# Performance work log

Measured on AMD Instinct MI355X. Metric: run time of the kernel, lower is better.

## Reference

```python
import jax, jax.numpy as jnp
import numpy as np

N_ITEMS = 100001  # n_items + 1 (padding idx 0)
D = 128           # item_embedding_dim == hidden_size
P = 3             # purposes
S, B = 100, 256   # seq_len, batch
TAU = 0.1
EPS = 0.01


def setup_inputs() -> dict:
    key = jax.random.key(0)
    ks = jax.random.split(key, 6)
    std = 1.0 / np.sqrt(D)
    seq = jax.random.randint(ks[0], (S, B), 0, N_ITEMS)          # [S, B] item ids
    lens = jax.random.randint(ks[1], (B,), 1, S + 1)             # valid lengths in [1, S]
    emb_table = jax.random.uniform(ks[2], (N_ITEMS, D), minval=-std, maxval=std, dtype=jnp.float32)
    purpose_table = jax.random.uniform(ks[3], (P, D), minval=-std, maxval=std, dtype=jnp.float32)
    x2h_w = jax.random.uniform(ks[4], (P, 3 * D, D), minval=-std, maxval=std, dtype=jnp.float32)  # 3 cells
    h2h_w = jax.random.uniform(ks[5], (P, 3 * D, D), minval=-std, maxval=std, dtype=jnp.float32)
    return {"seq": seq, "lens": lens, "emb_table": emb_table,
            "purpose_table": purpose_table, "x2h_w": x2h_w, "h2h_w": h2h_w}


def _psru_cell(x, h, concen, Wx, Wh):
    # x: [B,D], h: [B,D], concen: [B], Wx/Wh: [3D, D]
    gx = x @ Wx.T                              # [B, 3D]
    gh = h @ Wh.T                              # [B, 3D]
    i_r, i_i, i_n = jnp.split(gx, 3, axis=1)
    h_r, h_i, h_n = jnp.split(gh, 3, axis=1)
    resetgate = jax.nn.sigmoid(i_r + h_r)
    inputgate = jax.nn.sigmoid(i_i + h_i)
    newgate = jnp.tanh(i_n + resetgate * h_n)
    multi = jnp.where(concen >= EPS, concen, 0.0)[:, None] * inputgate
    return h + multi * (newgate - h)


def reference(seq, lens, emb_table, purpose_table, x2h_w, h2h_w):
    # padding_idx = 0
    emb_table = emb_table.at[0].set(0.0)
    # concentration matrix: softmax over purposes of normalized-embedding similarity / tau
    item_n = emb_table / jnp.clip(jnp.linalg.norm(emb_table, axis=1, keepdims=True), 1e-12)
    attr_n = purpose_table / jnp.clip(jnp.linalg.norm(purpose_table, axis=1, keepdims=True), 1e-12)
    g = jax.nn.softmax((item_n @ attr_n.T) / TAU, axis=1)   # [V, P]  (exp/sum == softmax)
    g = g.at[0].set(0.0)

    embs = emb_table[seq]        # [S, B, D]
    g_seq = g[seq]               # [S, B, P]

    h0 = jnp.zeros((P, B, D), emb_table.dtype)

    def step(h, xs):
        x, gq = xs  # x: [B,D], gq: [B,P]
        h_new = jnp.stack([_psru_cell(x, h[p], gq[:, p], x2h_w[p], h2h_w[p]) for p in range(P)])
        return h_new, h_new

    _, hs = jax.lax.scan(step, h0, (embs, g_seq))            # hs: [S, P, B, D]

    # select hidden at last valid step per example: outs[lens-1, arange(B)]
    h_last = hs[lens - 1, :, jnp.arange(B), :]               # [B, P, D]

    # delta_c[b,v] = sum_p g[v,p] * <h_last[b,p], item_n[v]>  (== original VC_cand * item_embs sum)
    logits = sum((h_last[:, p, :] @ item_n.T) * g[None, :, p] for p in range(P))  # [B, V]
    return jax.nn.sigmoid(logits)
```

## Files before the change

### kernel.cpp

```cpp
#include <hip/hip_runtime.h>
#include <hip/hip_bf16.h>
#include <math.h>

#define N_ITEMS 100001
#define DIM 128
#define NP 3
#define SEQ 100
#define NB 256
#define G3 384
#define TAU 0.1f
#define EPS_C 0.01f

#define OFF_G     0
#define OFF_C     300016
#define OFF_WXT   600032
#define OFF_WHT   747488
#define OFF_HLAST 894944
#define OFF_GX    993248
#define WS_FLOATS_PATHA (993248 + 29491200)

typedef float f32x4 __attribute__((ext_vector_type(4)));
typedef short s16x8 __attribute__((ext_vector_type(8)));
typedef unsigned int u32x4 __attribute__((ext_vector_type(4)));

__device__ __forceinline__ float sigmoidf_fast(float x) {
    return __builtin_amdgcn_rcpf(1.f + __builtin_amdgcn_exp2f(-1.4426950408889634f * x));
}
__device__ __forceinline__ float tanhf_fast(float x) {
    return 1.f - 2.f * __builtin_amdgcn_rcpf(1.f + __builtin_amdgcn_exp2f(2.8853900817779268f * x));
}
__device__ __forceinline__ unsigned short f2bf(float x) {
    union { float f; unsigned u; } v; v.f = x;
    unsigned r = v.u + 0x7fffu + ((v.u >> 16) & 1u);
    return (unsigned short)(r >> 16);
}
__device__ __forceinline__ float bf2f(unsigned short h) {
    union { unsigned u; float f; } v; v.u = ((unsigned)h) << 16;
    return v.f;
}
__device__ __forceinline__ unsigned cvt_pk_bf16(float a, float b) {
    unsigned r;
    asm("v_cvt_pk_bf16_f32 %0, %1, %2" : "=v"(r) : "v"(a), "v"(b));
    return r;
}

__global__ void k_prep_w(const float* __restrict__ x2h, const float* __restrict__ h2h,
                         float* __restrict__ wxT, float* __restrict__ whT) {
    int idx = blockIdx.x * 256 + threadIdx.x;
    if (idx >= NP * DIM * G3) return;
    int j = idx % G3;
    int k = (idx / G3) % DIM;
    int p = idx / (G3 * DIM);
    wxT[idx] = x2h[((size_t)p * G3 + j) * DIM + k];
    whT[idx] = h2h[((size_t)p * G3 + j) * DIM + k];
}

__global__ __launch_bounds__(256) void k_prep_wA(const float* __restrict__ x2h,
                                                 const float* __restrict__ h2h,
                                                 short* __restrict__ wxA_hi,
                                                 short* __restrict__ wxA_lo,
                                                 short* __restrict__ whA_hi,
                                                 short* __restrict__ whA_lo) {
    int e = blockIdx.x * 256 + threadIdx.x;
    if (e >= 2 * NP * 24 * 4 * 64) return;
    int which = (e >= NP * 24 * 4 * 64);
    int f = which ? e - NP * 24 * 4 * 64 : e;
    const float* tab = which ? h2h : x2h;
    short* dh = which ? whA_hi : wxA_hi;
    short* dl = which ? whA_lo : wxA_lo;
    int lane = f & 63;
    int ks = (f >> 6) & 3;
    int mt = (f >> 8) % 24;
    int p  = f / 6144;
    int j = mt * 16 + (lane & 15);
    int d = ks * 32 + (lane >> 4) * 8;
    const float* src = tab + ((size_t)p * G3 + j) * DIM + d;
    short hi[8], lo[8];
#pragma unroll
    for (int u = 0; u < 8; ++u) {
        float x = src[u];
        unsigned short h = f2bf(x);
        hi[u] = (short)h;
        lo[u] = (short)f2bf(x - bf2f(h));
    }
    *(s16x8*)(dh + (size_t)f * 8) = *(const s16x8*)hi;
    *(s16x8*)(dl + (size_t)f * 8) = *(const s16x8*)lo;
}

__global__ __launch_bounds__(256) void k_gc(const float* __restrict__ emb,
                                            const float* __restrict__ pt,
                                            float* __restrict__ g, float* __restrict__ c) {
    __shared__ float pt_l[G3];
    __shared__ float ainv[NP];
    int tid = threadIdx.x;
    for (int u = tid; u < G3; u += 256) pt_l[u] = pt[u];
    __syncthreads();
    if (tid < NP) {
        float ss = 0.f;
        for (int k = 0; k < DIM; ++k) { float v = pt_l[tid * DIM + k]; ss += v * v; }
        ainv[tid] = 1.f / fmaxf(sqrtf(ss), 1e-12f);
    }
    __syncthreads();
    int lane = tid & 63, wv = tid >> 6;
    for (int it = 0; it < 8; ++it) {
        int i = blockIdx.x * 32 + wv * 8 + it;
        if (i >= N_ITEMS) continue;
        float a = emb[(size_t)i * DIM + lane];
        float b = emb[(size_t)i * DIM + 64 + lane];
        float ss = a * a + b * b;
        float d0 = a * pt_l[lane]       + b * pt_l[64 + lane];
        float d1 = a * pt_l[128 + lane] + b * pt_l[192 + lane];
        float d2 = a * pt_l[256 + lane] + b * pt_l[320 + lane];
        for (int off = 32; off > 0; off >>= 1) {
            ss += __shfl_down(ss, off);
            d0 += __shfl_down(d0, off);
            d1 += __shfl_down(d1, off);
            d2 += __shfl_down(d2, off);
        }
        if (lane == 0) {
            if (i == 0) {
                g[0] = 0.f; g[1] = 0.f; g[2] = 0.f;
                c[0] = 0.f; c[1] = 0.f; c[2] = 0.f;
            } else {
                float inv = 1.f / fmaxf(sqrtf(ss), 1e-12f);
                float l0 = d0 * ainv[0] * inv * (1.f / TAU);
                float l1 = d1 * ainv[1] * inv * (1.f / TAU);
                float l2 = d2 * ainv[2] * inv * (1.f / TAU);
                float m = fmaxf(l0, fmaxf(l1, l2));
                float e0 = expf(l0 - m), e1 = expf(l1 - m), e2 = expf(l2 - m);
                float is = 1.f / (e0 + e1 + e2);
                float g0 = e0 * is, g1 = e1 * is, g2 = e2 * is;
                g[(size_t)i * 3 + 0] = g0; g[(size_t)i * 3 + 1] = g1; g[(size_t)i * 3 + 2] = g2;
                c[(size_t)i * 3 + 0] = g0 * inv; c[(size_t)i * 3 + 1] = g1 * inv; c[(size_t)i * 3 + 2] = g2 * inv;
            }
        }
    }
}

__global__ __launch_bounds__(512, 2) void k_gx_mfma(const int* __restrict__ seq,
                                                    const float* __restrict__ emb,
                                                    const short* __restrict__ wxA_hi,
                                                    const short* __restrict__ wxA_lo,
                                                    float* __restrict__ gx) {
    int bid = blockIdx.x;
    int t  = bid >> 4;
    int b0 = (bid & 15) * 16;
    int tid = threadIdx.x;
    int lane = tid & 63;
    int w = tid >> 6;
    int n = lane & 15;
    int q = lane >> 4;

    __shared__ int idx_l[16];
    __shared__ __align__(16) unsigned short xH[2048];
    __shared__ __align__(16) unsigned short xL[2048];

    if (tid < 16) idx_l[tid] = seq[t * NB + b0 + tid];
    __syncthreads();

    {
        int tk = tid >> 5, s = tid & 31;
        float4 v = *(const float4*)(emb + (size_t)idx_l[tk] * DIM + s * 4);
        int k = s * 4;
        int ks = k >> 5, km = k & 31;
        int ln = (km >> 3) * 16 + tk;
        int j0 = km & 7;
        int o = ks * 512 + ln * 8 + j0;
        float xv[4] = {v.x, v.y, v.z, v.w};
        unsigned short sh[4], sl[4];
#pragma unroll
        for (int r = 0; r < 4; ++r) {
            sh[r] = f2bf(xv[r]);
            sl[r] = f2bf(xv[r] - bf2f(sh[r]));
        }
        *(uint2*)(xH + o) = make_uint2((unsigned)sh[0] | ((unsigned)sh[1] << 16),
                                       (unsigned)sh[2] | ((unsigned)sh[3] << 16));
        *(uint2*)(xL + o) = make_uint2((unsigned)sl[0] | ((unsigned)sl[1] << 16),
                                       (unsigned)sl[2] | ((unsigned)sl[3] << 16));
    }
    __syncthreads();

    s16x8 bh[4], bl[4];
#pragma unroll
    for (int ks = 0; ks < 4; ++ks) {
        bh[ks] = ((const s16x8*)xH)[ks * 64 + lane];
        bl[ks] = ((const s16x8*)xL)[ks * 64 + lane];
    }

    float* gxt = gx + (size_t)(t * 3) * NB * G3;
#pragma unroll 3
    for (int ji = 0; ji < 9; ++ji) {
        int pid = w + ji * 8;
        int p = pid / 24, mt = pid % 24;
        f32x4 acc = {0.f, 0.f, 0.f, 0.f};
#pragma unroll
        for (int ks = 0; ks < 4; ++ks) {
            size_t ao = ((((size_t)p * 24 + mt) * 4 + ks) * 64 + lane) * 8;
            s16x8 ah = *(const s16x8*)(wxA_hi + ao);
            s16x8 al = *(const s16x8*)(wxA_lo + ao);
            acc = __builtin_amdgcn_mfma_f32_16x16x32_bf16(ah, bl[ks], acc, 0, 0, 0);
            acc = __builtin_amdgcn_mfma_f32_16x16x32_bf16(al, bh[ks], acc, 0, 0, 0);
            acc = __builtin_amdgcn_mfma_f32_16x16x32_bf16(ah, bh[ks], acc, 0, 0, 0);
        }
        float* o = gxt + ((size_t)p * NB + b0 + n) * G3 + mt * 16 + q * 4;
        *(float4*)o = make_float4(acc[0], acc[1], acc[2], acc[3]);
    }
}

__global__ __launch_bounds__(512, 2) void k_rnn3(const int* __restrict__ seq,
                                                 const int* __restrict__ lens,
                                                 const float* __restrict__ g,
                                                 const short* __restrict__ whA_hi,
                                                 const short* __restrict__ whA_lo,
                                                 const float* __restrict__ gx,
                                                 float* __restrict__ hlast) {
    int bid = blockIdx.x;
    int p  = bid / 16;
    int b0 = (bid % 16) * 16;
    int tid = threadIdx.x;
    int lane = tid & 63;
    int w = tid >> 6;
    int n = lane & 15;
    int q = lane >> 4;
    int d0 = w * 16 + q * 4;

    __shared__ __align__(16) unsigned short hH[2 * 2048];
    __shared__ __align__(16) unsigned short hL[2 * 2048];
    __shared__ float conc_s[SEQ * 16];

    for (int u = tid; u < 2048; u += 512) { hH[u] = 0; hL[u] = 0; }

    for (int e = tid; e < SEQ * 16; e += 512) {
        int t = e >> 4, b = e & 15;
        int ix = seq[t * NB + b0 + b];
        float cc = g[(size_t)ix * 3 + p];
        conc_s[e] = (cc >= EPS_C) ? cc : 0.f;
    }

    s16x8 whH[3][4], whL[3][4];
    int mts0 = w, mts1 = 8 + w, mts2 = 16 + w;
#pragma unroll
    for (int ks = 0; ks < 4; ++ks) {
        size_t o0 = ((((size_t)p * 24 + mts0) * 4 + ks) * 64 + lane) * 8;
        size_t o1 = ((((size_t)p * 24 + mts1) * 4 + ks) * 64 + lane) * 8;
        size_t o2 = ((((size_t)p * 24 + mts2) * 4 + ks) * 64 + lane) * 8;
        whH[0][ks] = *(const s16x8*)(whA_hi + o0);
        whH[1][ks] = *(const s16x8*)(whA_hi + o1);
        whH[2][ks] = *(const s16x8*)(whA_hi + o2);
        whL[0][ks] = *(const s16x8*)(whA_lo + o0);
        whL[1][ks] = *(const s16x8*)(whA_lo + o1);
        whL[2][ks] = *(const s16x8*)(whA_lo + o2);
    }

    int len_n = lens[b0 + n];
    float h0 = 0.f, h1 = 0.f, h2 = 0.f, h3 = 0.f;

    int wks = d0 >> 5;
    int km  = d0 & 31;
    int rl  = (km >> 3) * 16 + n;
    int jj0 = km & 7;
    int widx = wks * 512 + rl * 8 + jj0;

    const float* gxbase = gx + ((size_t)p * NB + (b0 + n)) * G3 + d0;
    const size_t tstride = (size_t)3 * NB * G3;

    f32x4 pgr = *(const f32x4*)(gxbase);
    f32x4 pgi = *(const f32x4*)(gxbase + DIM);
    f32x4 pgn = *(const f32x4*)(gxbase + 2 * DIM);

    __syncthreads();

    int cur = 0;
    for (int t = 0; t < SEQ; ++t) {
        f32x4 grv = pgr, giv = pgi, gnv = pgn;
        int tn = (t + 1 < SEQ) ? (t + 1) : t;
        const float* gp = gxbase + (size_t)tn * tstride;
        pgr = *(const f32x4*)(gp);
        pgi = *(const f32x4*)(gp + DIM);
        pgn = *(const f32x4*)(gp + 2 * DIM);

        float cc = conc_s[t * 16 + n];

        f32x4 acc0 = {0.f,0.f,0.f,0.f}, acc1 = {0.f,0.f,0.f,0.f}, acc2 = {0.f,0.f,0.f,0.f};
        const s16x8* bhp = (const s16x8*)hH + cur * 256 + lane;
        const s16x8* blp = (const s16x8*)hL + cur * 256 + lane;
#pragma unroll
        for (int ks = 0; ks < 4; ++ks) {
            s16x8 bh = bhp[ks * 64];
            s16x8 bl = blp[ks * 64];
            acc0 = __builtin_amdgcn_mfma_f32_16x16x32_bf16(whH[0][ks], bl, acc0, 0, 0, 0);
            acc1 = __builtin_amdgcn_mfma_f32_16x16x32_bf16(whH[1][ks], bl, acc1, 0, 0, 0);
            acc2 = __builtin_amdgcn_mfma_f32_16x16x32_bf16(whH[2][ks], bl, acc2, 0, 0, 0);
            acc0 = __builtin_amdgcn_mfma_f32_16x16x32_bf16(whL[0][ks], bh, acc0, 0, 0, 0);
            acc1 = __builtin_amdgcn_mfma_f32_16x16x32_bf16(whL[1][ks], bh, acc1, 0, 0, 0);
            acc2 = __builtin_amdgcn_mfma_f32_16x16x32_bf16(whL[2][ks], bh, acc2, 0, 0, 0);
            acc0 = __builtin_amdgcn_mfma_f32_16x16x32_bf16(whH[0][ks], bh, acc0, 0, 0, 0);
            acc1 = __builtin_amdgcn_mfma_f32_16x16x32_bf16(whH[1][ks], bh, acc1, 0, 0, 0);
            acc2 = __builtin_amdgcn_mfma_f32_16x16x32_bf16(whH[2][ks], bh, acc2, 0, 0, 0);
        }

        float ar[4], ai[4], an[4], gr4[4], gi4[4], gn4[4];
        *(f32x4*)ar = acc0; *(f32x4*)ai = acc1; *(f32x4*)an = acc2;
        *(f32x4*)gr4 = grv; *(f32x4*)gi4 = giv; *(f32x4*)gn4 = gnv;
        float hh[4] = {h0, h1, h2, h3};
        float hnew[4];
#pragma unroll
        for (int r = 0; r < 4; ++r) {
            float rr = sigmoidf_fast(gr4[r] + ar[r]);
            float ig = sigmoidf_fast(gi4[r] + ai[r]);
            float ng = tanhf_fast(gn4[r] + rr * an[r]);
            float m2 = cc * ig;
            hnew[r] = hh[r] + m2 * (ng - hh[r]);
        }
        h0 = hnew[0]; h1 = hnew[1]; h2 = hnew[2]; h3 = hnew[3];

        if (t == len_n - 1) {
            float* hp = hlast + (size_t)(b0 + n) * G3 + p * DIM + d0;
            *(float4*)hp = make_float4(h0, h1, h2, h3);
        }

        unsigned sh01 = cvt_pk_bf16(hnew[0], hnew[1]);
        unsigned sh23 = cvt_pk_bf16(hnew[2], hnew[3]);
        union { unsigned u; float f; } r0, r1, r2, r3;
        r0.u = sh01 << 16;        r1.u = sh01 & 0xffff0000u;
        r2.u = sh23 << 16;        r3.u = sh23 & 0xffff0000u;
        unsigned sl01 = cvt_pk_bf16(hnew[0] - r0.f, hnew[1] - r1.f);
        unsigned sl23 = cvt_pk_bf16(hnew[2] - r2.f, hnew[3] - r3.f);
        int wb = (cur ^ 1) * 2048 + widx;
        *(uint2*)(hH + wb) = make_uint2(sh01, sh23);
        *(uint2*)(hL + wb) = make_uint2(sl01, sl23);

        asm volatile("s_waitcnt lgkmcnt(0)" ::: "memory");
        __builtin_amdgcn_sched_barrier(0);
        __builtin_amdgcn_s_barrier();
        __builtin_amdgcn_sched_barrier(0);
        cur ^= 1;
    }
}

__global__ __launch_bounds__(384) void k_rnn(const int* __restrict__ seq,
                                             const int* __restrict__ lens,
                                             const float* __restrict__ emb,
                                             const float* __restrict__ g,
                                             const float* __restrict__ wxT,
                                             const float* __restrict__ whT,
                                             float* __restrict__ hlast) {
    int bid = blockIdx.x;
    int b0 = (bid & 63) * 4;
    int p = bid >> 6;
    __shared__ __align__(16) float h_l[DIM * 4];
    __shared__ __align__(16) float x_l[DIM * 4];
    __shared__ __align__(16) float sx_l[G3 * 4];
    __shared__ __align__(16) float sh_l[G3 * 4];
    __shared__ float conc_l[4];
    __shared__ int idx_l[4];
    __shared__ int len_l[4];
    int tid = threadIdx.x;
    if (tid < 4) len_l[tid] = lens[b0 + tid];
    for (int u = tid; u < DIM * 4; u += 384) h_l[u] = 0.f;
    __syncthreads();
    const float* wh = whT + (size_t)p * (DIM * G3);
    const float* wx = wxT + (size_t)p * (DIM * G3);
    for (int t = 0; t < SEQ; ++t) {
        if (tid < 4) {
            int ix = seq[t * NB + b0 + tid];
            idx_l[tid] = ix;
            conc_l[tid] = g[(size_t)ix * 3 + p];
        }
        __syncthreads();
        for (int u = tid; u < DIM * 4; u += 384) {
            int bc = u >> 7, k = u & 127;
            x_l[k * 4 + bc] = emb[(size_t)idx_l[bc] * DIM + k];
        }
        __syncthreads();
        int j = tid;
        float ax0 = 0.f, ax1 = 0.f, ax2 = 0.f, ax3 = 0.f;
#pragma unroll 4
        for (int k = 0; k < DIM; ++k) {
            float wv = wx[(size_t)k * G3 + j];
            float4 xv = *(const float4*)(x_l + k * 4);
            ax0 += wv * xv.x; ax1 += wv * xv.y; ax2 += wv * xv.z; ax3 += wv * xv.w;
        }
        float ah0 = 0.f, ah1 = 0.f, ah2 = 0.f, ah3 = 0.f;
#pragma unroll 4
        for (int k = 0; k < DIM; ++k) {
            float wv = wh[(size_t)k * G3 + j];
            float4 hv = *(const float4*)(h_l + k * 4);
            ah0 += wv * hv.x; ah1 += wv * hv.y; ah2 += wv * hv.z; ah3 += wv * hv.w;
        }
        *(float4*)(sx_l + j * 4) = make_float4(ax0, ax1, ax2, ax3);
        *(float4*)(sh_l + j * 4) = make_float4(ah0, ah1, ah2, ah3);
        __syncthreads();
        for (int u = tid; u < DIM * 4; u += 384) {
            int bc = u & 3, d = u >> 2;
            float sr = sx_l[d * 4 + bc] + sh_l[d * 4 + bc];
            float si = sx_l[(DIM + d) * 4 + bc] + sh_l[(DIM + d) * 4 + bc];
            float xn = sx_l[(2 * DIM + d) * 4 + bc];
            float hn = sh_l[(2 * DIM + d) * 4 + bc];
            float r  = sigmoidf_fast(sr);
            float ig = sigmoidf_fast(si);
            float ng = tanhf_fast(xn + r * hn);
            float h  = h_l[d * 4 + bc];
            float cc = conc_l[bc];
            float multi = (cc >= EPS_C ? cc : 0.f) * ig;
            float hnew = h + multi * (ng - h);
            h_l[d * 4 + bc] = hnew;
            if (t == len_l[bc] - 1)
                hlast[(size_t)(b0 + bc) * G3 + p * DIM + d] = hnew;
        }
        __syncthreads();
    }
}

__global__ __launch_bounds__(256) void k_prep_h(const float* __restrict__ hlast,
                                                short* __restrict__ hl_hi,
                                                short* __restrict__ hl_lo) {
    int e = blockIdx.x * 256 + threadIdx.x;
    int b = e / G3;
    int k = e % G3;
    float x = hlast[e];
    unsigned short hi = f2bf(x);
    unsigned short lo = f2bf(x - bf2f(hi));
    int off = (k >> 5) * 8192 + b * 32 + ((k >> 3) & 3) * 8 + (k & 7);
    hl_hi[off] = (short)hi;
    hl_lo[off] = (short)lo;
}

__global__ __launch_bounds__(256) void k_logits_mfma(const float* __restrict__ emb,
                                                     const float* __restrict__ c,
                                                     const short* __restrict__ hl_hi,
                                                     const short* __restrict__ hl_lo,
                                                     float* __restrict__ out) {
    int i0 = blockIdx.x * 64;
    int tid = threadIdx.x;
    int w = tid >> 6;
    int lane = tid & 63;
    int n = lane & 15;
    int q = lane >> 4;

    __shared__ __align__(16) float embs[64 * 132];

    for (int u = tid; u < 64 * 32; u += 256) {
        int i = u >> 5;
        int s = u & 31;
        int gi = i0 + i;
        float4 v = make_float4(0.f, 0.f, 0.f, 0.f);
        if (gi < N_ITEMS) v = *(const float4*)(emb + (size_t)gi * DIM + s * 4);
        *(float4*)(embs + i * 132 + s * 4) = v;
    }

    float cv[4][3];
#pragma unroll
    for (int is = 0; is < 4; ++is) {
        int gi = i0 + is * 16 + n;
#pragma unroll
        for (int p = 0; p < 3; ++p)
            cv[is][p] = (gi < N_ITEMS) ? c[(size_t)gi * 3 + p] : 0.f;
    }
    __syncthreads();

    f32x4 acc[4][4];
#pragma unroll
    for (int bs = 0; bs < 4; ++bs)
#pragma unroll
        for (int is = 0; is < 4; ++is)
            acc[bs][is] = (f32x4){0.f, 0.f, 0.f, 0.f};

    for (int ks = 0; ks < 12; ++ks) {
        int p = ks >> 2;
        int d0 = (ks & 3) * 32;
        int abase = ks * 8192 + (w * 64 + n) * 32 + q * 8;
        s16x8 ah[4], al[4];
#pragma unroll
        for (int bs = 0; bs < 4; ++bs) {
            ah[bs] = *(const s16x8*)(hl_hi + abase + bs * 512);
            al[bs] = *(const s16x8*)(hl_lo + abase + bs * 512);
        }
#pragma unroll
        for (int is = 0; is < 4; ++is) {
            const float* src = embs + (is * 16 + n) * 132 + d0 + q * 8;
            float x[8];
            *(float4*)(x)     = *(const float4*)(src);
            *(float4*)(x + 4) = *(const float4*)(src + 4);
            float sc = cv[is][p];
            union { u32x4 u; s16x8 s; } bh_, bl_;
#pragma unroll
            for (int jp = 0; jp < 4; ++jp) {
                float a = x[2 * jp]     * sc;
                float b = x[2 * jp + 1] * sc;
                unsigned hp = cvt_pk_bf16(a, b);
                union { unsigned u; float f; } ba, bb;
                ba.u = hp << 16;
                bb.u = hp & 0xffff0000u;
                unsigned lp = cvt_pk_bf16(a - ba.f, b - bb.f);
                bh_.u[jp] = hp;
                bl_.u[jp] = lp;
            }
            s16x8 bhv = bh_.s;
            s16x8 blv = bl_.s;
#pragma unroll
            for (int bs = 0; bs < 4; ++bs) {
                acc[bs][is] = __builtin_amdgcn_mfma_f32_16x16x32_bf16(ah[bs], blv, acc[bs][is], 0, 0, 0);
                acc[bs][is] = __builtin_amdgcn_mfma_f32_16x16x32_bf16(al[bs], bhv, acc[bs][is], 0, 0, 0);
                acc[bs][is] = __builtin_amdgcn_mfma_f32_16x16x32_bf16(ah[bs], bhv, acc[bs][is], 0, 0, 0);
            }
        }
    }

#pragma unroll
    for (int is = 0; is < 4; ++is) {
        int gi = i0 + is * 16 + n;
        if (gi >= N_ITEMS) continue;
#pragma unroll
        for (int bs = 0; bs < 4; ++bs) {
            int brow = w * 64 + bs * 16 + q * 4;
#pragma unroll
            for (int r = 0; r < 4; ++r)
                out[(size_t)(brow + r) * N_ITEMS + gi] = sigmoidf_fast(acc[bs][is][r]);
        }
    }
}

extern "C" void kernel_launch(void* const* d_in, const int* in_sizes, int n_in,
                              void* d_out, int out_size, void* d_ws, size_t ws_size,
                              hipStream_t stream) {
    const int*   seq  = (const int*)d_in[0];
    const int*   lens = (const int*)d_in[1];
    const float* emb  = (const float*)d_in[2];
    const float* pt   = (const float*)d_in[3];
    const float* x2h  = (const float*)d_in[4];
    const float* h2h  = (const float*)d_in[5];
    float* out = (float*)d_out;
    float* ws  = (float*)d_ws;

    float* g     = ws + OFF_G;
    float* c     = ws + OFF_C;
    float* wxT   = ws + OFF_WXT;
    float* whT   = ws + OFF_WHT;
    float* hlast = ws + OFF_HLAST;
    float* gxbuf = ws + OFF_GX;
    short* wxA_hi = (short*)(ws + OFF_WXT);
    short* wxA_lo = wxA_hi + 147456;
    short* whA_hi = (short*)(ws + OFF_WHT);
    short* whA_lo = whA_hi + 147456;
    short* hl_hi = (short*)(ws + OFF_GX);
    short* hl_lo = hl_hi + 98304;

    int useGx = (ws_size >= (size_t)WS_FLOATS_PATHA * 4) ? 1 : 0;

    k_gc<<<3126, 256, 0, stream>>>(emb, pt, g, c);
    if (useGx) {
        k_prep_wA<<<144, 256, 0, stream>>>(x2h, h2h, wxA_hi, wxA_lo, whA_hi, whA_lo);
        k_gx_mfma<<<1600, 512, 0, stream>>>(seq, emb, wxA_hi, wxA_lo, gxbuf);
        k_rnn3<<<48, 512, 0, stream>>>(seq, lens, g, whA_hi, whA_lo, gxbuf, hlast);
    } else {
        k_prep_w<<<576, 256, 0, stream>>>(x2h, h2h, wxT, whT);
        k_rnn<<<192, 384, 0, stream>>>(seq, lens, emb, g, wxT, whT, hlast);
    }
    k_prep_h<<<384, 256, 0, stream>>>(hlast, hl_hi, hl_lo);
    k_logits_mfma<<<1563, 256, 0, stream>>>(emb, c, hl_hi, hl_lo, out);
}
```

Baseline: 403.3 us.

## Pack two batch tiles per RNN block and split K-chain into two accumulators

Result: slower. 761.3 us (+88.8%).

```diff
diff --git a/kernel.cpp b/kernel.cpp
--- a/kernel.cpp
+++ b/kernel.cpp
@@ -207,32 +207,35 @@
     }
 }
 
-__global__ __launch_bounds__(512, 2) void k_rnn3(const int* __restrict__ seq,
-                                                 const int* __restrict__ lens,
-                                                 const float* __restrict__ g,
-                                                 const short* __restrict__ whA_hi,
-                                                 const short* __restrict__ whA_lo,
-                                                 const float* __restrict__ gx,
-                                                 float* __restrict__ hlast) {
+__global__ __launch_bounds__(1024, 4) void k_rnn3(const int* __restrict__ seq,
+                                                  const int* __restrict__ lens,
+                                                  const float* __restrict__ g,
+                                                  const short* __restrict__ whA_hi,
+                                                  const short* __restrict__ whA_lo,
+                                                  const float* __restrict__ gx,
+                                                  float* __restrict__ hlast) {
     int bid = blockIdx.x;
-    int p  = bid / 16;
-    int b0 = (bid % 16) * 16;
+    int p  = bid / 8;
+    int bg = bid % 8;
     int tid = threadIdx.x;
+    int tile2 = tid >> 9;
+    int tl  = tid & 511;
     int lane = tid & 63;
-    int w = tid >> 6;
+    int w = tl >> 6;
     int n = lane & 15;
     int q = lane >> 4;
     int d0 = w * 16 + q * 4;
-
-    __shared__ __align__(16) unsigned short hH[2 * 2048];
-    __shared__ __align__(16) unsigned short hL[2 * 2048];
-    __shared__ float conc_s[SEQ * 16];
-
-    for (int u = tid; u < 2048; u += 512) { hH[u] = 0; hL[u] = 0; }
-
-    for (int e = tid; e < SEQ * 16; e += 512) {
-        int t = e >> 4, b = e & 15;
-        int ix = seq[t * NB + b0 + b];
+    int b0 = bg * 32 + tile2 * 16;
+
+    __shared__ __align__(16) unsigned short hH[2 * 4096];
+    __shared__ __align__(16) unsigned short hL[2 * 4096];
+    __shared__ float conc_s[SEQ * 32];
+
+    for (int u = tid; u < 4096; u += 1024) { hH[u] = 0; hL[u] = 0; }
+
+    for (int e = tid; e < SEQ * 32; e += 1024) {
+        int t = e >> 5, b = e & 31;
+        int ix = seq[t * NB + bg * 32 + b];
         float cc = g[(size_t)ix * 3 + p];
         conc_s[e] = (cc >= EPS_C) ? cc : 0.f;
     }
@@ -279,25 +282,43 @@
         pgi = *(const f32x4*)(gp + DIM);
         pgn = *(const f32x4*)(gp + 2 * DIM);
 
-        float cc = conc_s[t * 16 + n];
-
-        f32x4 acc0 = {0.f,0.f,0.f,0.f}, acc1 = {0.f,0.f,0.f,0.f}, acc2 = {0.f,0.f,0.f,0.f};
-        const s16x8* bhp = (const s16x8*)hH + cur * 256 + lane;
-        const s16x8* blp = (const s16x8*)hL + cur * 256 + lane;
-#pragma unroll
-        for (int ks = 0; ks < 4; ++ks) {
+        float cc = conc_s[t * 32 + tile2 * 16 + n];
+
+        f32x4 a0A = {0.f,0.f,0.f,0.f}, a1A = {0.f,0.f,0.f,0.f}, a2A = {0.f,0.f,0.f,0.f};
+        f32x4 a0B = {0.f,0.f,0.f,0.f}, a1B = {0.f,0.f,0.f,0.f}, a2B = {0.f,0.f,0.f,0.f};
+        const s16x8* bhp = (const s16x8*)hH + cur * 512 + tile2 * 256 + lane;
+        const s16x8* blp = (const s16x8*)hL + cur * 512 + tile2 * 256 + lane;
+#pragma unroll
+        for (int ks = 0; ks < 2; ++ks) {
             s16x8 bh = bhp[ks * 64];
             s16x8 bl = blp[ks * 64];
-            acc0 = __builtin_amdgcn_mfma_f32_16x16x32_bf16(whH[0][ks], bl, acc0, 0, 0, 0);
-            acc1 = __builtin_amdgcn_mfma_f32_16x16x32_bf16(whH[1][ks], bl, acc1, 0, 0, 0);
-            acc2 = __builtin_amdgcn_mfma_f32_16x16x32_bf16(whH[2][ks], bl, acc2, 0, 0, 0);
-            acc0 = __builtin_amdgcn_mfma_f32_16x16x32_bf16(whL[0][ks], bh, acc0, 0, 0, 0);
-            acc1 = __builtin_amdgcn_mfma_f32_16x16x32_bf16(whL[1][ks], bh, acc1, 0, 0, 0);
-            acc2 = __builtin_amdgcn_mfma_f32_16x16x32_bf16(whL[2][ks], bh, acc2, 0, 0, 0);
-            acc0 = __builtin_amdgcn_mfma_f32_16x16x32_bf16(whH[0][ks], bh, acc0, 0, 0, 0);
-            acc1 = __builtin_amdgcn_mfma_f32_16x16x32_bf16(whH[1][ks], bh, acc1, 0, 0, 0);
-            acc2 = __builtin_amdgcn_mfma_f32_16x16x32_bf16(whH[2][ks], bh, acc2, 0, 0, 0);
-        }
+            a0A = __builtin_amdgcn_mfma_f32_16x16x32_bf16(whH[0][ks], bl, a0A, 0, 0, 0);
+            a1A = __builtin_amdgcn_mfma_f32_16x16x32_bf16(whH[1][ks], bl, a1A, 0, 0, 0);
+            a2A = __builtin_amdgcn_mfma_f32_16x16x32_bf16(whH[2][ks], bl, a2A, 0, 0, 0);
+            a0A = __builtin_amdgcn_mfma_f32_16x16x32_bf16(whL[0][ks], bh, a0A, 0, 0, 0);
+            a1A = __builtin_amdgcn_mfma_f32_16x16x32_bf16(whL[1][ks], bh, a1A, 0, 0, 0);
+            a2A = __builtin_amdgcn_mfma_f32_16x16x32_bf16(whL[2][ks], bh, a2A, 0, 0, 0);
+            a0A = __builtin_amdgcn_mfma_f32_16x16x32_bf16(whH[0][ks], bh, a0A, 0, 0, 0);
+            a1A = __builtin_amdgcn_mfma_f32_16x16x32_bf16(whH[1][ks], bh, a1A, 0, 0, 0);
+            a2A = __builtin_amdgcn_mfma_f32_16x16x32_bf16(whH[2][ks], bh, a2A, 0, 0, 0);
+        }
+#pragma unroll
+        for (int ks = 2; ks < 4; ++ks) {
+            s16x8 bh = bhp[ks * 64];
+            s16x8 bl = blp[ks * 64];
+            a0B = __builtin_amdgcn_mfma_f32_16x16x32_bf16(whH[0][ks], bl, a0B, 0, 0, 0);
+            a1B = __builtin_amdgcn_mfma_f32_16x16x32_bf16(whH[1][ks], bl, a1B, 0, 0, 0);
+            a2B = __builtin_amdgcn_mfma_f32_16x16x32_bf16(whH[2][ks], bl, a2B, 0, 0, 0);
+            a0B = __builtin_amdgcn_mfma_f32_16x16x32_bf16(whL[0][ks], bh, a0B, 0, 0, 0);
+            a1B = __builtin_amdgcn_mfma_f32_16x16x32_bf16(whL[1][ks], bh, a1B, 0, 0, 0);
+            a2B = __builtin_amdgcn_mfma_f32_16x16x32_bf16(whL[2][ks], bh, a2B, 0, 0, 0);
+            a0B = __builtin_amdgcn_mfma_f32_16x16x32_bf16(whH[0][ks], bh, a0B, 0, 0, 0);
+            a1B = __builtin_amdgcn_mfma_f32_16x16x32_bf16(whH[1][ks], bh, a1B, 0, 0, 0);
+            a2B = __builtin_amdgcn_mfma_f32_16x16x32_bf16(whH[2][ks], bh, a2B, 0, 0, 0);
+        }
+        f32x4 acc0 = a0A + a0B;
+        f32x4 acc1 = a1A + a1B;
+        f32x4 acc2 = a2A + a2B;
 
         float ar[4], ai[4], an[4], gr4[4], gi4[4], gn4[4];
         *(f32x4*)ar = acc0; *(f32x4*)ai = acc1; *(f32x4*)an = acc2;
@@ -321,12 +342,12 @@
 
         unsigned sh01 = cvt_pk_bf16(hnew[0], hnew[1]);
         unsigned sh23 = cvt_pk_bf16(hnew[2], hnew[3]);
-        union { unsigned u; float f; } r0, r1, r2, r3;
-        r0.u = sh01 << 16;        r1.u = sh01 & 0xffff0000u;
-        r2.u = sh23 << 16;        r3.u = sh23 & 0xffff0000u;
+        union { unsigned uu; float f; } r0, r1, r2, r3;
+        r0.uu = sh01 << 16;        r1.uu = sh01 & 0xffff0000u;
+        r2.uu = sh23 << 16;        r3.uu = sh23 & 0xffff0000u;
         unsigned sl01 = cvt_pk_bf16(hnew[0] - r0.f, hnew[1] - r1.f);
         unsigned sl23 = cvt_pk_bf16(hnew[2] - r2.f, hnew[3] - r3.f);
-        int wb = (cur ^ 1) * 2048 + widx;
+        int wb = (cur ^ 1) * 4096 + tile2 * 2048 + widx;
         *(uint2*)(hH + wb) = make_uint2(sh01, sh23);
         *(uint2*)(hL + wb) = make_uint2(sl01, sl23);
 
@@ -552,7 +573,7 @@
     if (useGx) {
         k_prep_wA<<<144, 256, 0, stream>>>(x2h, h2h, wxA_hi, wxA_lo, whA_hi, whA_lo);
         k_gx_mfma<<<1600, 512, 0, stream>>>(seq, emb, wxA_hi, wxA_lo, gxbuf);
-        k_rnn3<<<48, 512, 0, stream>>>(seq, lens, g, whA_hi, whA_lo, gxbuf, hlast);
+        k_rnn3<<<24, 1024, 0, stream>>>(seq, lens, g, whA_hi, whA_lo, gxbuf, hlast);
     } else {
         k_prep_w<<<576, 256, 0, stream>>>(x2h, h2h, wxT, whT);
         k_rnn<<<192, 384, 0, stream>>>(seq, lens, emb, g, wxT, whT, hlast);
```
